# Optimization experiments

Hardware: AMD Instinct MI355X
Metric: run time of the kernel (lower is better)

Reference implementation:

```python
import jax, jax.numpy as jnp
import numpy as np

DIM = 2048
N_HEADS = 32
N_KV_HEADS = 8
HEAD_DIM = 64
REPEATS = N_HEADS // N_KV_HEADS
SCALE = HEAD_DIM ** -0.5
L = 2048
B = 1


def rotary_matrix(context_len, d):
    # Dense (L, d, d) RoPE rotation matrix, exactly as get_rotary_matrix1.
    pos = jnp.arange(1, context_len + 1, dtype=jnp.float32)[:, None]
    i = jnp.arange(d // 2)
    theta = 10000.0 ** (-2.0 * i.astype(jnp.float32) / d)
    m_theta = pos * theta  # (L, d/2)
    cos_v, sin_v = jnp.cos(m_theta), jnp.sin(m_theta)
    R = jnp.zeros((context_len, d, d), dtype=jnp.float32)
    R = R.at[:, 2 * i, 2 * i].set(cos_v)
    R = R.at[:, 2 * i, 2 * i + 1].set(-sin_v)
    R = R.at[:, 2 * i + 1, 2 * i].set(sin_v)
    R = R.at[:, 2 * i + 1, 2 * i + 1].set(cos_v)
    return R


def causal_mask(context_len):
    idx = jnp.arange(context_len)
    return (idx[:, None] < idx[None, :]).astype(jnp.float32) * -1e9


def setup_inputs() -> dict:
    key = jax.random.key(0)
    ks = jax.random.split(key, 5)
    x = jax.random.normal(ks[0], (B, L, DIM), dtype=jnp.float32)
    mask = causal_mask(L)
    wq_w = jax.random.normal(ks[1], (N_HEADS * HEAD_DIM, DIM), dtype=jnp.float32) * 0.02
    wk_w = jax.random.normal(ks[2], (N_KV_HEADS * HEAD_DIM, DIM), dtype=jnp.float32) * 0.02
    wv_w = jax.random.normal(ks[3], (N_KV_HEADS * HEAD_DIM, DIM), dtype=jnp.float32) * 0.02
    wo_w = jax.random.normal(ks[4], (DIM, N_HEADS * HEAD_DIM), dtype=jnp.float32) * 0.02
    return {"x": x, "mask": mask, "wq_w": wq_w, "wk_w": wk_w, "wv_w": wv_w, "wo_w": wo_w}


def reference(x, mask, wq_w, wk_w, wv_w, wo_w):
    Bx, Lx, D = x.shape
    # projections (torch Linear: y = x @ W.T)
    q = jnp.einsum('bld,od->blo', x, wq_w).reshape(Bx, Lx, N_HEADS, HEAD_DIM).transpose(0, 2, 1, 3)
    k = jnp.einsum('bld,od->blo', x, wk_w).reshape(Bx, Lx, N_KV_HEADS, HEAD_DIM).transpose(0, 2, 1, 3)
    v = jnp.einsum('bld,od->blo', x, wv_w).reshape(Bx, Lx, N_KV_HEADS, HEAD_DIM).transpose(0, 2, 1, 3)
    # GQA repeat of kv heads (interleaved, matching concat-unsqueeze-reshape)
    k = jnp.repeat(k, REPEATS, axis=1)
    v = jnp.repeat(v, REPEATS, axis=1)
    # dense-matrix RoPE on q and (repeated) k
    R = rotary_matrix(Lx, HEAD_DIM)
    q = jnp.einsum('bhlj,lij->bhli', q, R)
    k = jnp.einsum('bhlj,lij->bhli', k, R)
    scores = jnp.einsum('bhld,bhmd->bhlm', q, k) * SCALE + mask
    attn = jax.nn.softmax(scores.astype(jnp.float32), axis=-1)
    out = jnp.einsum('bhlm,bhmd->bhld', attn, v)
    out = out.transpose(0, 2, 1, 3).reshape(Bx, Lx, N_HEADS * HEAD_DIM)
    out = jnp.einsum('blo,do->bld', out, wo_w)
    return out, k, v
```

## Files before the change

### kernel.cpp

```cpp
#include <hip/hip_runtime.h>

typedef __bf16 bf16;
typedef __bf16 bf16x8 __attribute__((ext_vector_type(8)));
typedef float floatx4 __attribute__((ext_vector_type(4)));
typedef float floatx16 __attribute__((ext_vector_type(16)));
typedef unsigned int uint;

#define MFMA16(a, b, c) __builtin_amdgcn_mfma_f32_16x16x32_bf16((a), (b), (c), 0, 0, 0)
#define MFMA32(a, b, c) __builtin_amdgcn_mfma_f32_32x32x16_bf16((a), (b), (c), 0, 0, 0)

__device__ __forceinline__ void gl2lds16(const bf16* g, bf16* l) {
  __builtin_amdgcn_global_load_lds(
      (const __attribute__((address_space(1))) void*)g,
      (__attribute__((address_space(3))) void*)l, 16, 0, 0);
}
__device__ __forceinline__ void wait_vm0() { __builtin_amdgcn_s_waitcnt(0x0f70); }

__device__ __forceinline__ float* slot_ptr(int s, float* o0, float* o1) {
  return s < 512 ? o0 + (size_t)s * 8192 : o1 + (size_t)(s - 512) * 8192;
}
__device__ __forceinline__ const float* slot_ptr_c(int s, const float* o0,
                                                   const float* o1) {
  return s < 512 ? o0 + (size_t)s * 8192 : o1 + (size_t)(s - 512) * 8192;
}

__device__ __forceinline__ void cvt8(const float* __restrict__ s,
                                     bf16* __restrict__ d, int i8) {
  const float4 a = ((const float4*)s)[i8 * 2];
  const float4 b = ((const float4*)s)[i8 * 2 + 1];
  bf16x8 o;
  o[0] = (bf16)a.x; o[1] = (bf16)a.y; o[2] = (bf16)a.z; o[3] = (bf16)a.w;
  o[4] = (bf16)b.x; o[5] = (bf16)b.y; o[6] = (bf16)b.z; o[7] = (bf16)b.w;
  *(bf16x8*)(d + i8 * 8) = o;
}

__global__ __launch_bounds__(256) void convert_kernel(
    const float* __restrict__ x, const float* __restrict__ wq,
    const float* __restrict__ wk, const float* __restrict__ wv,
    bf16* __restrict__ xb, bf16* __restrict__ wqb, bf16* __restrict__ wkb,
    bf16* __restrict__ wvb) {
  const int g = blockIdx.x * 256 + threadIdx.x;
  if (g < 524288) cvt8(x, xb, g);
  else if (g < 1048576) cvt8(wq, wqb, g - 524288);
  else if (g < 1179648) cvt8(wk, wkb, g - 1048576);
  else cvt8(wv, wvb, g - 1179648);
}

template <typename OutT>
__device__ __forceinline__ void gemm_tile_body64(
    const bf16* __restrict__ A, int lda,
    const bf16* __restrict__ B, int ldb,
    OutT* __restrict__ C, int ldc, int K,
    bf16* S) {
  const int t = threadIdx.x;
  const int w = t >> 6, lane = t & 63;
  const int l15 = lane & 15, qd = lane >> 4;
  const int wr = w >> 1, wc = w & 1;

  floatx4 acc[2][4];
#pragma unroll
  for (int i = 0; i < 2; ++i)
#pragma unroll
    for (int j = 0; j < 4; ++j) acc[i][j] = (floatx4){0.f, 0.f, 0.f, 0.f};

  const bf16* gb[6];
  int lo[6];
#pragma unroll
  for (int i = 0; i < 6; ++i) {
    const int u = w + 4 * i;
    lo[i] = u * 512 + lane * 8;
    if (u < 8) {
      gb[i] = A + ((u >> 1) * 16 + l15) * lda + (u & 1) * 32 + qd * 8;
    } else {
      const int v = u - 8;
      gb[i] = B + ((v >> 1) * 16 + l15) * ldb + (v & 1) * 32 + qd * 8;
    }
  }

#define STG64(kt_, buf_)                                            \
  {                                                                 \
    bf16* d_ = S + (buf_) * 12288;                                  \
    _Pragma("unroll")                                               \
    for (int i_ = 0; i_ < 6; ++i_)                                  \
      gl2lds16(gb[i_] + (kt_) * 64, d_ + lo[i_]);                   \
  }

  const int NT = K >> 6;
  STG64(0, 0);
  wait_vm0();
  __syncthreads();
  int cur = 0;
  for (int kt = 0; kt < NT; ++kt) {
    if (kt + 1 < NT) STG64(kt + 1, cur ^ 1);
    const bf16* Ab = S + cur * 12288;
    const bf16* Bb = Ab + 4096;
    bf16x8 a[2][2], b[4][2];
#pragma unroll
    for (int i = 0; i < 2; ++i)
#pragma unroll
      for (int kk = 0; kk < 2; ++kk)
        a[i][kk] =
            *(const bf16x8*)(Ab + ((wr * 2 + i) * 2 + kk) * 512 + lane * 8);
#pragma unroll
    for (int j = 0; j < 4; ++j)
#pragma unroll
      for (int kk = 0; kk < 2; ++kk)
        b[j][kk] =
            *(const bf16x8*)(Bb + ((wc * 4 + j) * 2 + kk) * 512 + lane * 8);
#pragma unroll
    for (int kk = 0; kk < 2; ++kk)
#pragma unroll
      for (int i = 0; i < 2; ++i)
#pragma unroll
        for (int j = 0; j < 4; ++j)
          acc[i][j] = MFMA16(a[i][kk], b[j][kk], acc[i][j]);
    wait_vm0();
    __builtin_amdgcn_sched_barrier(0);
    __builtin_amdgcn_s_barrier();
    __builtin_amdgcn_sched_barrier(0);
    cur ^= 1;
  }
#undef STG64

#pragma unroll
  for (int i = 0; i < 2; ++i)
#pragma unroll
    for (int j = 0; j < 4; ++j) {
      const int row = wr * 32 + i * 16 + qd * 4;
      const int col = wc * 64 + j * 16 + l15;
#pragma unroll
      for (int r = 0; r < 4; ++r)
        C[(row + r) * ldc + col] = (OutT)acc[i][j][r];
    }
}

__global__ __launch_bounds__(256) void gemm_qkv(
    const bf16* __restrict__ x, const bf16* __restrict__ wq,
    const bf16* __restrict__ wk, const bf16* __restrict__ wv,
    bf16* __restrict__ Qws, bf16* __restrict__ Kh, bf16* __restrict__ Vh,
    bf16* __restrict__ Vt) {
  __shared__ bf16 SM[17152];
  bf16* As = SM;
  bf16* Bs = SM + 8192;
  const int bid = blockIdx.y * 24 + blockIdx.x;
  const int swz = (bid & 7) * 48 + (bid >> 3);
  const int nb = swz % 24;
  const int m0 = (swz / 24) * 128;
  const bf16* B;
  if (nb < 16) B = wq + nb * 128 * 2048;
  else if (nb < 20) B = wk + (nb - 16) * 128 * 2048;
  else B = wv + (nb - 20) * 128 * 2048;

  const int t = threadIdx.x;
  const int w = t >> 6, lane = t & 63;
  const int l15 = lane & 15, qd = lane >> 4;
  const int wr = w >> 1, wc = w & 1;

  floatx4 acc[4][4];
#pragma unroll
  for (int i = 0; i < 4; ++i)
#pragma unroll
    for (int j = 0; j < 4; ++j) acc[i][j] = (floatx4){0.f, 0.f, 0.f, 0.f};

  const bf16* A = x + m0 * 2048;
  const int mt0 = w, mt1 = w + 4;
  const int kseg = qd * 8;
  const bf16* ga0 = A + (mt0 * 16 + l15) * 2048 + kseg;
  const bf16* ga1 = A + (mt1 * 16 + l15) * 2048 + kseg;
  const bf16* gb0 = B + (mt0 * 16 + l15) * 2048 + kseg;
  const bf16* gb1 = B + (mt1 * 16 + l15) * 2048 + kseg;
  bf16* lA00 = As + (mt0 * 2 + 0) * 512 + lane * 8;
  bf16* lA01 = As + (mt0 * 2 + 1) * 512 + lane * 8;
  bf16* lA10 = As + (mt1 * 2 + 0) * 512 + lane * 8;
  bf16* lA11 = As + (mt1 * 2 + 1) * 512 + lane * 8;
  bf16* lB00 = Bs + (mt0 * 2 + 0) * 512 + lane * 8;
  bf16* lB01 = Bs + (mt0 * 2 + 1) * 512 + lane * 8;
  bf16* lB10 = Bs + (mt1 * 2 + 0) * 512 + lane * 8;
  bf16* lB11 = Bs + (mt1 * 2 + 1) * 512 + lane * 8;

  for (int k0 = 0; k0 < 2048; k0 += 64) {
    gl2lds16(ga0 + k0, lA00);
    gl2lds16(ga0 + k0 + 32, lA01);
    gl2lds16(ga1 + k0, lA10);
    gl2lds16(ga1 + k0 + 32, lA11);
    gl2lds16(gb0 + k0, lB00);
    gl2lds16(gb0 + k0 + 32, lB01);
    gl2lds16(gb1 + k0, lB10);
    gl2lds16(gb1 + k0 + 32, lB11);
    wait_vm0();
    __syncthreads();

    bf16x8 a[4][2], b[4][2];
#pragma unroll
    for (int i = 0; i < 4; ++i)
#pragma unroll
      for (int kk = 0; kk < 2; ++kk)
        a[i][kk] =
            *(const bf16x8*)(As + ((wr * 4 + i) * 2 + kk) * 512 + lane * 8);
#pragma unroll
    for (int j = 0; j < 4; ++j)
#pragma unroll
      for (int kk = 0; kk < 2; ++kk)
        b[j][kk] =
            *(const bf16x8*)(Bs + ((wc * 4 + j) * 2 + kk) * 512 + lane * 8);
#pragma unroll
    for (int kk = 0; kk < 2; ++kk)
#pragma unroll
      for (int i = 0; i < 4; ++i)
#pragma unroll
        for (int j = 0; j < 4; ++j)
          acc[i][j] = MFMA16(a[i][kk], b[j][kk], acc[i][j]);
    __syncthreads();
  }

#pragma unroll
  for (int i = 0; i < 4; ++i)
#pragma unroll
    for (int j = 0; j < 4; ++j) {
      const int row = wr * 64 + i * 16 + qd * 4;
      const int col = wc * 64 + j * 16 + l15;
#pragma unroll
      for (int r = 0; r < 4; ++r)
        SM[(row + r) * 134 + col] = (bf16)acc[i][j][r];
    }
  __syncthreads();

  const float NEG_LOG2_10000_D32 = -0.4152410118609203f;
  if (nb < 16) {
#pragma unroll
    for (int k = 0; k < 8; ++k) {
      const int u = t + (k << 8);
      const int row = u >> 4, c8 = (u & 15) << 3;
      const bf16x8 v = *(const bf16x8*)&SM[row * 134 + c8];
      const float base = (float)(m0 + row + 1);
      bf16x8 ov;
#pragma unroll
      for (int p = 0; p < 4; ++p) {
        const int a = ((c8 & 63) >> 1) + p;
        float s, c;
        __sincosf(base * exp2f(NEG_LOG2_10000_D32 * (float)a), &s, &c);
        const float x0 = (float)v[2 * p], x1 = (float)v[2 * p + 1];
        ov[2 * p] = (bf16)(c * x0 - s * x1);
        ov[2 * p + 1] = (bf16)(s * x0 + c * x1);
      }
      *(bf16x8*)&Qws[(m0 + row) * 2048 + nb * 128 + c8] = ov;
    }
  } else if (nb < 20) {
#pragma unroll
    for (int k = 0; k < 8; ++k) {
      const int u = t + (k << 8);
      const int row = u >> 4, c8 = (u & 15) << 3;
      const bf16x8 v = *(const bf16x8*)&SM[row * 134 + c8];
      const float base = (float)(m0 + row + 1);
      bf16x8 ov;
#pragma unroll
      for (int p = 0; p < 4; ++p) {
        const int a = ((c8 & 63) >> 1) + p;
        float s, c;
        __sincosf(base * exp2f(NEG_LOG2_10000_D32 * (float)a), &s, &c);
        const float x0 = (float)v[2 * p], x1 = (float)v[2 * p + 1];
        ov[2 * p] = (bf16)(c * x0 - s * x1);
        ov[2 * p + 1] = (bf16)(s * x0 + c * x1);
      }
      const int g512 = (nb - 16) * 128 + c8;
      const int kvh = g512 >> 6, d8 = g512 & 63;
      *(bf16x8*)&Kh[(kvh * 2048 + m0 + row) * 64 + d8] = ov;
    }
  } else {
#pragma unroll
    for (int k = 0; k < 8; ++k) {
      const int u = t + (k << 8);
      const int row = u >> 4, c8 = (u & 15) << 3;
      const bf16x8 v = *(const bf16x8*)&SM[row * 134 + c8];
      const int g512 = (nb - 20) * 128 + c8;
      const int kvh = g512 >> 6, d8 = g512 & 63;
      *(bf16x8*)&Vh[(kvh * 2048 + m0 + row) * 64 + d8] = v;
    }
#pragma unroll
    for (int k = 0; k < 8; ++k) {
      const int u = t + (k << 8);
      const int col = u >> 4, r8 = (u & 15) << 3;
      bf16x8 v;
#pragma unroll
      for (int jj = 0; jj < 8; ++jj) v[jj] = SM[(r8 + jj) * 134 + col];
      const int g512 = (nb - 20) * 128 + col;
      const int kvh = g512 >> 6, d = g512 & 63;
      *(bf16x8*)&Vt[kvh * 131072 + d * 2048 + m0 + r8] = v;
    }
  }
}

__global__ __launch_bounds__(256) void gemm_o(
    const bf16* __restrict__ Ows, const bf16* __restrict__ wo,
    float* __restrict__ out, const bf16* __restrict__ Kh,
    const bf16* __restrict__ Vh, float* __restrict__ kout,
    float* __restrict__ vout) {
  __shared__ bf16 S[24576];
  const int bid = blockIdx.y * 16 + blockIdx.x;
  const int swz = (bid & 7) * 64 + (bid >> 3);
  const int n0 = (swz & 15) * 128;
  const int m0 = (swz >> 4) * 64;
  gemm_tile_body64<float>(Ows + m0 * 2048, 2048, wo + n0 * 2048, 2048,
                          out + m0 * 2048 + n0, 2048, 2048, S);

  const int g = bid * 256 + (int)threadIdx.x;
  for (uint u = (uint)g; u < 262144u; u += 131072u) {
    const uint u2 = u & 131071u;
    const bf16* src = (u < 131072u) ? Kh : Vh;
    float* dst = (u < 131072u) ? kout : vout;
    const int kvh2 = u2 >> 14;
    const int rr = u2 & 16383;
    const int l = rr >> 3, d8 = (rr & 7) * 8;
    const bf16x8 v = *(const bf16x8*)(src + (kvh2 * 2048 + l) * 64 + d8);
    float4 f0, f1;
    f0.x = (float)v[0]; f0.y = (float)v[1]; f0.z = (float)v[2]; f0.w = (float)v[3];
    f1.x = (float)v[4]; f1.y = (float)v[5]; f1.z = (float)v[6]; f1.w = (float)v[7];
#pragma unroll
    for (int rep = 0; rep < 4; ++rep) {
      float* o2 = dst + (((kvh2 * 4 + rep) * 2048 + l) * 64 + d8);
      *(float4*)o2 = f0;
      *(float4*)(o2 + 4) = f1;
    }
  }
}

__global__ __launch_bounds__(256) void flash_kernel(
    const bf16* __restrict__ Qws, const bf16* __restrict__ Kh,
    const bf16* __restrict__ Vt, bf16* __restrict__ Ows,
    float* __restrict__ Op0, float* __restrict__ Op1, float* __restrict__ ML,
    const float* __restrict__ wo, bf16* __restrict__ wob) {
  __shared__ bf16 SMEM[16384];

  const int h = blockIdx.y;
  const int bx = 35 - (int)blockIdx.x;
  int qt, seg, kts, kte, slot;
  if (bx < 4) {
    qt = bx; seg = -1; kts = 0; kte = 2 * qt + 2; slot = -1;
  } else if (bx < 12) {
    const int j = bx - 4;
    qt = 4 + (j >> 1); seg = j & 1;
    const int nkt = 2 * qt + 2;
    kts = seg * nkt / 2; kte = (seg + 1) * nkt / 2;
    slot = h * 32 + (bx - 4);
  } else {
    const int j = bx - 12;
    qt = 8 + j / 3; seg = j % 3;
    const int nkt = 2 * qt + 2;
    kts = seg * nkt / 3; kte = (seg + 1) * nkt / 3;
    slot = h * 32 + (bx - 4);
  }
  const int kh = h >> 2;
  const int q0 = qt * 128;
  const int t = threadIdx.x, w = t >> 6, lane = t & 63;
  const int l31 = lane & 31, hf = lane >> 5;
  const int qw = q0 + w * 32;

  const int s0 = w, s1 = w + 4;
  const bf16* gK0 = Kh + kh * 131072 + ((s0 >> 2) * 32 + l31) * 64 + (s0 & 3) * 16 + hf * 8;
  const bf16* gK1 = Kh + kh * 131072 + ((s1 >> 2) * 32 + l31) * 64 + (s1 & 3) * 16 + hf * 8;
  const bf16* gV0 = Vt + kh * 131072 + ((s0 >> 2) * 32 + l31) * 2048 + (s0 & 3) * 16 + hf * 8;
  const bf16* gV1 = Vt + kh * 131072 + ((s1 >> 2) * 32 + l31) * 2048 + (s1 & 3) * 16 + hf * 8;

  {
    const int nb = kts & 1;
    gl2lds16(gK0 + kts * 4096, &SMEM[nb * 8192 + s0 * 512 + lane * 8]);
    gl2lds16(gK1 + kts * 4096, &SMEM[nb * 8192 + s1 * 512 + lane * 8]);
    gl2lds16(gV0 + kts * 64, &SMEM[nb * 8192 + 4096 + s0 * 512 + lane * 8]);
    gl2lds16(gV1 + kts * 64, &SMEM[nb * 8192 + 4096 + s1 * 512 + lane * 8]);
  }

  bf16x8 qf[4];
  {
    const bf16* qrow = Qws + (qw + l31) * 2048 + h * 64 + hf * 8;
#pragma unroll
    for (int c = 0; c < 4; ++c) qf[c] = *(const bf16x8*)(qrow + c * 16);
  }

  floatx16 o[2] = {};
  float mrun = -3e38f, lrun = 0.f;

  const float C = 0.1803368801f;
  for (int kt = kts; kt < kte; ++kt) {
    wait_vm0();
    __syncthreads();
    if (kt + 1 < kte) {
      const int nb = (kt + 1) & 1;
      const int koff = (kt + 1) * 4096, voff = (kt + 1) * 64;
      gl2lds16(gK0 + koff, &SMEM[nb * 8192 + s0 * 512 + lane * 8]);
      gl2lds16(gK1 + koff, &SMEM[nb * 8192 + s1 * 512 + lane * 8]);
      gl2lds16(gV0 + voff, &SMEM[nb * 8192 + 4096 + s0 * 512 + lane * 8]);
      gl2lds16(gV1 + voff, &SMEM[nb * 8192 + 4096 + s1 * 512 + lane * 8]);
    }
    const int kt64 = kt * 64;
    if (kt64 > qw + 31) continue;
    const bf16* Kb = &SMEM[(kt & 1) * 8192];
    const bf16* Vb = Kb + 4096;

    floatx16 st[2];
    __builtin_amdgcn_s_setprio(1);
#pragma unroll
    for (int tt = 0; tt < 2; ++tt) {
      floatx16 z = {};
#pragma unroll
      for (int c = 0; c < 4; ++c) {
        const bf16x8 kf = *(const bf16x8*)(Kb + (tt * 4 + c) * 512 + lane * 8);
        z = MFMA32(kf, qf[c], z);
      }
      st[tt] = z;
    }
    __builtin_amdgcn_s_setprio(0);
    if (kt64 + 64 > qw) {
      const int myq = qw + l31;
#pragma unroll
      for (int tt = 0; tt < 2; ++tt)
#pragma unroll
        for (int r = 0; r < 16; ++r) {
          const int key = kt64 + tt * 32 + (r & 3) + 8 * (r >> 2) + 4 * hf;
          if (key > myq) st[tt][r] = -1e30f;
        }
    }
    float ma = -3e38f, mb = -3e38f, mc = -3e38f, md = -3e38f;
#pragma unroll
    for (int tt = 0; tt < 2; ++tt)
#pragma unroll
      for (int r = 0; r < 16; r += 4) {
        ma = fmaxf(ma, st[tt][r + 0]);
        mb = fmaxf(mb, st[tt][r + 1]);
        mc = fmaxf(mc, st[tt][r + 2]);
        md = fmaxf(md, st[tt][r + 3]);
      }
    float mx = fmaxf(fmaxf(ma, mb), fmaxf(mc, md));
    mx = fmaxf(mx, __shfl_xor(mx, 32));
    const bool defer = __all((mx - mrun) * C <= 8.f);
    if (!defer) {
      const float mn = fmaxf(mrun, mx);
      const float al = __builtin_amdgcn_exp2f((mrun - mn) * C);
      lrun *= al;
#pragma unroll
      for (int n = 0; n < 2; ++n)
#pragma unroll
        for (int r = 0; r < 16; ++r) o[n][r] *= al;
      mrun = mn;
    }
    float ra = 0.f, rb = 0.f, rc = 0.f, rd = 0.f;
#pragma unroll
    for (int tt = 0; tt < 2; ++tt)
#pragma unroll
      for (int r = 0; r < 16; r += 4) {
        const float p0 = __builtin_amdgcn_exp2f((st[tt][r + 0] - mrun) * C);
        const float p1 = __builtin_amdgcn_exp2f((st[tt][r + 1] - mrun) * C);
        const float p2 = __builtin_amdgcn_exp2f((st[tt][r + 2] - mrun) * C);
        const float p3 = __builtin_amdgcn_exp2f((st[tt][r + 3] - mrun) * C);
        st[tt][r + 0] = p0; ra += p0;
        st[tt][r + 1] = p1; rb += p1;
        st[tt][r + 2] = p2; rc += p2;
        st[tt][r + 3] = p3; rd += p3;
      }
    float rs = (ra + rb) + (rc + rd);
    rs += __shfl_xor(rs, 32);
    lrun += rs;

    uint pk[2][4][2];
#pragma unroll
    for (int tt = 0; tt < 2; ++tt)
#pragma unroll
      for (int g = 0; g < 4; ++g)
#pragma unroll
        for (int p = 0; p < 2; ++p) {
          union { bf16 h2[2]; uint u; } cv;
          cv.h2[0] = (bf16)st[tt][4 * g + 2 * p];
          cv.h2[1] = (bf16)st[tt][4 * g + 2 * p + 1];
          pk[tt][g][p] = cv.u;
        }
    uint own_[2][2][2], rv[2][2][2];
#pragma unroll
    for (int tt = 0; tt < 2; ++tt)
#pragma unroll
      for (int gam = 0; gam < 2; ++gam)
#pragma unroll
        for (int p = 0; p < 2; ++p) {
          own_[tt][gam][p] = hf ? pk[tt][2 * gam + 1][p] : pk[tt][2 * gam][p];
          const uint snd = hf ? pk[tt][2 * gam][p] : pk[tt][2 * gam + 1][p];
          rv[tt][gam][p] = (uint)__shfl_xor((int)snd, 32);
        }
    __builtin_amdgcn_s_setprio(1);
#pragma unroll
    for (int c = 0; c < 4; ++c) {
      const int tt = c >> 1, gam = c & 1;
      union { uint u[4]; bf16x8 v; } pf;
      pf.u[0] = hf ? rv[tt][gam][0] : own_[tt][gam][0];
      pf.u[1] = hf ? rv[tt][gam][1] : own_[tt][gam][1];
      pf.u[2] = hf ? own_[tt][gam][0] : rv[tt][gam][0];
      pf.u[3] = hf ? own_[tt][gam][1] : rv[tt][gam][1];
#pragma unroll
      for (int n = 0; n < 2; ++n)
        o[n] = MFMA32(*(const bf16x8*)(Vb + (n * 4 + c) * 512 + lane * 8),
                      pf.v, o[n]);
    }
    __builtin_amdgcn_s_setprio(0);
  }

  if (seg < 0) {
    __syncthreads();
    bf16* Osh = SMEM;
    const float inv = 1.f / lrun;
#pragma unroll
    for (int n = 0; n < 2; ++n)
#pragma unroll
      for (int r = 0; r < 16; ++r) {
        const int dl = n * 32 + (r & 3) + 8 * (r >> 2) + 4 * hf;
        Osh[(w * 32 + l31) * 66 + dl] = (bf16)(o[n][r] * inv);
      }
    __syncthreads();
#pragma unroll
    for (int i = 0; i < 4; ++i) {
      const int row = (t >> 3) + i * 32;
      const int col = (t & 7) * 8;
      const bf16x8 vv = *(const bf16x8*)&Osh[row * 66 + col];
      *(bf16x8*)&Ows[(q0 + row) * 2048 + h * 64 + col] = vv;
    }
  } else {
    float* Op = slot_ptr(slot, Op0, Op1);
#pragma unroll
    for (int n = 0; n < 2; ++n)
#pragma unroll
      for (int r = 0; r < 16; ++r) {
        const int dl = n * 32 + (r & 3) + 8 * (r >> 2) + 4 * hf;
        Op[dl * 128 + w * 32 + l31] = o[n][r];
      }
    if (hf == 0) {
      ML[slot * 256 + w * 32 + l31] = mrun;
      ML[slot * 256 + 128 + w * 32 + l31] = lrun;
    }
  }

  {
    const int bidf = (int)blockIdx.y * 36 + (int)blockIdx.x;
    for (uint u = (uint)(bidf * 256 + t); u < 524288u; u += 294912u)
      cvt8(wo, wob, (int)u);
  }
}

__global__ __launch_bounds__(256) void combine_kernel(
    const float* __restrict__ Op0, const float* __restrict__ Op1,
    const float* __restrict__ ML, bf16* __restrict__ Ows) {
  __shared__ bf16 Osh[128 * 66];
  const int b = blockIdx.x;
  const int h = b / 12, qi = b % 12;
  const int qt = 4 + qi;
  const int q0 = qt * 128;
  const bool three = (qi >= 4);
  const int slot0 = h * 32 + (three ? 8 + (qi - 4) * 3 : qi * 2);
  const int t = threadIdx.x;
  const int row = t & 127, dh = t >> 7;
  const float C = 0.1803368801f;
  const float m0 = ML[(slot0 + 0) * 256 + row], l0 = ML[(slot0 + 0) * 256 + 128 + row];
  const float m1 = ML[(slot0 + 1) * 256 + row], l1 = ML[(slot0 + 1) * 256 + 128 + row];
  const float m2 = three ? ML[(slot0 + 2) * 256 + row] : -3e38f;
  const float l2 = three ? ML[(slot0 + 2) * 256 + 128 + row] : 0.f;
  const float m = fmaxf(fmaxf(m0, m1), m2);
  const float w0 = __builtin_amdgcn_exp2f((m0 - m) * C);
  const float w1 = __builtin_amdgcn_exp2f((m1 - m) * C);
  const float w2 = three ? __builtin_amdgcn_exp2f((m2 - m) * C) : 0.f;
  const float inv = 1.f / (l0 * w0 + l1 * w1 + l2 * w2);
  const float* P0 = slot_ptr_c(slot0 + 0, Op0, Op1);
  const float* P1 = slot_ptr_c(slot0 + 1, Op0, Op1);
  const float* P2 = three ? slot_ptr_c(slot0 + 2, Op0, Op1) : P0;
#pragma unroll
  for (int j = 0; j < 32; ++j) {
    const int d = dh * 32 + j;
    const float v = (P0[d * 128 + row] * w0 + P1[d * 128 + row] * w1 +
                     P2[d * 128 + row] * w2) *
                    inv;
    Osh[row * 66 + d] = (bf16)v;
  }
  __syncthreads();
#pragma unroll
  for (int i = 0; i < 4; ++i) {
    const int r2 = (t >> 3) + i * 32;
    const int col = (t & 7) * 8;
    const bf16x8 vv = *(const bf16x8*)&Osh[r2 * 66 + col];
    *(bf16x8*)&Ows[(q0 + r2) * 2048 + h * 64 + col] = vv;
  }
}

extern "C" void kernel_launch(void* const* d_in, const int* in_sizes, int n_in,
                              void* d_out, int out_size, void* d_ws,
                              size_t ws_size, hipStream_t stream) {
  const float* x = (const float*)d_in[0];
  const float* wq = (const float*)d_in[2];
  const float* wk = (const float*)d_in[3];
  const float* wv = (const float*)d_in[4];
  const float* wo = (const float*)d_in[5];

  float* out = (float*)d_out;
  float* kout = out + 4194304;
  float* vout = out + 8388608;

  bf16* ws = (bf16*)d_ws;
  bf16* xb = ws;
  bf16* wqb = xb + 4194304;
  bf16* wkb = wqb + 4194304;
  bf16* wvb = wkb + 1048576;
  bf16* wob = wvb + 1048576;
  bf16* Qws = wob + 4194304;
  bf16* Kws = Qws + 4194304;
  bf16* Vh = Kws + 1048576;
  bf16* Vt = Vh + 1048576;
  bf16* Ows = Vt + 1048576;
  bf16* Kh = Ows + 4194304;
  float* Op0 = out;
  float* Op1 = (float*)ws;
  float* MLf = (float*)Kws;

  convert_kernel<<<dim3(5120), dim3(256), 0, stream>>>(x, wq, wk, wv, xb, wqb,
                                                       wkb, wvb);
  gemm_qkv<<<dim3(24, 16), dim3(256), 0, stream>>>(xb, wqb, wkb, wvb, Qws, Kh,
                                                   Vh, Vt);
  flash_kernel<<<dim3(36, 32), dim3(256), 0, stream>>>(Qws, Kh, Vt, Ows, Op0,
                                                       Op1, MLf, wo, wob);
  combine_kernel<<<dim3(384), dim3(256), 0, stream>>>(Op0, Op1, MLf, Ows);
  gemm_o<<<dim3(16, 32), dim3(256), 0, stream>>>(Ows, wob, out, Kh, Vh, kout,
                                                 vout);
}
```

Before: 277.9 us.

## Fuse split-K combine into flash kernel via last-block atomic counter

Removes the separate combine kernel: each split segment block increments a per-(head, query tile) atomic counter after writing its partial output and max/sum stats. The last block to arrive reads all partials and writes the normalized bf16 output. Counters are reset in the convert kernel. This saves a kernel launch and the gap between kernels, at the cost of threadfences, an atomic, and serial combine work in the tail blocks.

```diff
diff --git a/kernel.cpp b/kernel.cpp
--- a/kernel.cpp
+++ b/kernel.cpp
@@ -38,12 +38,15 @@
     const float* __restrict__ x, const float* __restrict__ wq,
     const float* __restrict__ wk, const float* __restrict__ wv,
     bf16* __restrict__ xb, bf16* __restrict__ wqb, bf16* __restrict__ wkb,
-    bf16* __restrict__ wvb) {
+    bf16* __restrict__ wvb, uint* __restrict__ cnt) {
   const int g = blockIdx.x * 256 + threadIdx.x;
   if (g < 524288) cvt8(x, xb, g);
   else if (g < 1048576) cvt8(wq, wqb, g - 524288);
   else if (g < 1179648) cvt8(wk, wkb, g - 1048576);
   else cvt8(wv, wvb, g - 1179648);
+  if (blockIdx.x == 0) {
+    for (int i = threadIdx.x; i < 384; i += 256) cnt[i] = 0u;
+  }
 }
 
 template <typename OutT>
@@ -328,23 +331,25 @@
     const bf16* __restrict__ Qws, const bf16* __restrict__ Kh,
     const bf16* __restrict__ Vt, bf16* __restrict__ Ows,
     float* __restrict__ Op0, float* __restrict__ Op1, float* __restrict__ ML,
-    const float* __restrict__ wo, bf16* __restrict__ wob) {
+    uint* __restrict__ cnt, const float* __restrict__ wo,
+    bf16* __restrict__ wob) {
   __shared__ bf16 SMEM[16384];
+  __shared__ int s_last;
 
   const int h = blockIdx.y;
   const int bx = 35 - (int)blockIdx.x;
-  int qt, seg, kts, kte, slot;
+  int qt, seg, kts, kte, slot, nseg;
   if (bx < 4) {
-    qt = bx; seg = -1; kts = 0; kte = 2 * qt + 2; slot = -1;
+    qt = bx; seg = -1; kts = 0; kte = 2 * qt + 2; slot = -1; nseg = 1;
   } else if (bx < 12) {
     const int j = bx - 4;
-    qt = 4 + (j >> 1); seg = j & 1;
+    qt = 4 + (j >> 1); seg = j & 1; nseg = 2;
     const int nkt = 2 * qt + 2;
     kts = seg * nkt / 2; kte = (seg + 1) * nkt / 2;
     slot = h * 32 + (bx - 4);
   } else {
     const int j = bx - 12;
-    qt = 8 + j / 3; seg = j % 3;
+    qt = 8 + j / 3; seg = j % 3; nseg = 3;
     const int nkt = 2 * qt + 2;
     kts = seg * nkt / 3; kte = (seg + 1) * nkt / 3;
     slot = h * 32 + (bx - 4);
@@ -532,55 +537,59 @@
       ML[slot * 256 + w * 32 + l31] = mrun;
       ML[slot * 256 + 128 + w * 32 + l31] = lrun;
     }
+
+    const int qi = qt - 4;
+    const int cidx = h * 12 + qi;
+    __threadfence();
+    __syncthreads();
+    if (t == 0) {
+      const uint old = atomicAdd(&cnt[cidx], 1u);
+      s_last = (old == (uint)(nseg - 1)) ? 1 : 0;
+    }
+    __syncthreads();
+    if (s_last) {
+      __threadfence();
+      const bool three = (nseg == 3);
+      const int slot0 = h * 32 + (three ? 8 + qi * 3 - 12 : qi * 2);
+      const int row = t & 127, dh = t >> 7;
+      const float m0_ = ML[(slot0 + 0) * 256 + row];
+      const float l0_ = ML[(slot0 + 0) * 256 + 128 + row];
+      const float m1_ = ML[(slot0 + 1) * 256 + row];
+      const float l1_ = ML[(slot0 + 1) * 256 + 128 + row];
+      const float m2_ = three ? ML[(slot0 + 2) * 256 + row] : -3e38f;
+      const float l2_ = three ? ML[(slot0 + 2) * 256 + 128 + row] : 0.f;
+      const float m = fmaxf(fmaxf(m0_, m1_), m2_);
+      const float w0_ = __builtin_amdgcn_exp2f((m0_ - m) * C);
+      const float w1_ = __builtin_amdgcn_exp2f((m1_ - m) * C);
+      const float w2_ = three ? __builtin_amdgcn_exp2f((m2_ - m) * C) : 0.f;
+      const float inv = 1.f / (l0_ * w0_ + l1_ * w1_ + l2_ * w2_);
+      const float* P0 = slot_ptr_c(slot0 + 0, Op0, Op1);
+      const float* P1 = slot_ptr_c(slot0 + 1, Op0, Op1);
+      const float* P2 = three ? slot_ptr_c(slot0 + 2, Op0, Op1) : P0;
+      bf16* Osh = SMEM;
+#pragma unroll
+      for (int j = 0; j < 32; ++j) {
+        const int d = dh * 32 + j;
+        const float v = (P0[d * 128 + row] * w0_ + P1[d * 128 + row] * w1_ +
+                         P2[d * 128 + row] * w2_) *
+                        inv;
+        Osh[row * 66 + d] = (bf16)v;
+      }
+      __syncthreads();
+#pragma unroll
+      for (int i = 0; i < 4; ++i) {
+        const int r2 = (t >> 3) + i * 32;
+        const int col = (t & 7) * 8;
+        const bf16x8 vv = *(const bf16x8*)&Osh[r2 * 66 + col];
+        *(bf16x8*)&Ows[(q0 + r2) * 2048 + h * 64 + col] = vv;
+      }
+    }
   }
 
   {
     const int bidf = (int)blockIdx.y * 36 + (int)blockIdx.x;
     for (uint u = (uint)(bidf * 256 + t); u < 524288u; u += 294912u)
       cvt8(wo, wob, (int)u);
-  }
-}
-
-__global__ __launch_bounds__(256) void combine_kernel(
-    const float* __restrict__ Op0, const float* __restrict__ Op1,
-    const float* __restrict__ ML, bf16* __restrict__ Ows) {
-  __shared__ bf16 Osh[128 * 66];
-  const int b = blockIdx.x;
-  const int h = b / 12, qi = b % 12;
-  const int qt = 4 + qi;
-  const int q0 = qt * 128;
-  const bool three = (qi >= 4);
-  const int slot0 = h * 32 + (three ? 8 + (qi - 4) * 3 : qi * 2);
-  const int t = threadIdx.x;
-  const int row = t & 127, dh = t >> 7;
-  const float C = 0.1803368801f;
-  const float m0 = ML[(slot0 + 0) * 256 + row], l0 = ML[(slot0 + 0) * 256 + 128 + row];
-  const float m1 = ML[(slot0 + 1) * 256 + row], l1 = ML[(slot0 + 1) * 256 + 128 + row];
-  const float m2 = three ? ML[(slot0 + 2) * 256 + row] : -3e38f;
-  const float l2 = three ? ML[(slot0 + 2) * 256 + 128 + row] : 0.f;
-  const float m = fmaxf(fmaxf(m0, m1), m2);
-  const float w0 = __builtin_amdgcn_exp2f((m0 - m) * C);
-  const float w1 = __builtin_amdgcn_exp2f((m1 - m) * C);
-  const float w2 = three ? __builtin_amdgcn_exp2f((m2 - m) * C) : 0.f;
-  const float inv = 1.f / (l0 * w0 + l1 * w1 + l2 * w2);
-  const float* P0 = slot_ptr_c(slot0 + 0, Op0, Op1);
-  const float* P1 = slot_ptr_c(slot0 + 1, Op0, Op1);
-  const float* P2 = three ? slot_ptr_c(slot0 + 2, Op0, Op1) : P0;
-#pragma unroll
-  for (int j = 0; j < 32; ++j) {
-    const int d = dh * 32 + j;
-    const float v = (P0[d * 128 + row] * w0 + P1[d * 128 + row] * w1 +
-                     P2[d * 128 + row] * w2) *
-                    inv;
-    Osh[row * 66 + d] = (bf16)v;
-  }
-  __syncthreads();
-#pragma unroll
-  for (int i = 0; i < 4; ++i) {
-    const int r2 = (t >> 3) + i * 32;
-    const int col = (t & 7) * 8;
-    const bf16x8 vv = *(const bf16x8*)&Osh[r2 * 66 + col];
-    *(bf16x8*)&Ows[(q0 + r2) * 2048 + h * 64 + col] = vv;
   }
 }
 
@@ -612,14 +621,14 @@
   float* Op0 = out;
   float* Op1 = (float*)ws;
   float* MLf = (float*)Kws;
+  uint* cnt = (uint*)(MLf + 262144);
 
   convert_kernel<<<dim3(5120), dim3(256), 0, stream>>>(x, wq, wk, wv, xb, wqb,
-                                                       wkb, wvb);
+                                                       wkb, wvb, cnt);
   gemm_qkv<<<dim3(24, 16), dim3(256), 0, stream>>>(xb, wqb, wkb, wvb, Qws, Kh,
                                                    Vh, Vt);
   flash_kernel<<<dim3(36, 32), dim3(256), 0, stream>>>(Qws, Kh, Vt, Ows, Op0,
-                                                       Op1, MLf, wo, wob);
-  combine_kernel<<<dim3(384), dim3(256), 0, stream>>>(Op0, Op1, MLf, Ows);
+                                                       Op1, MLf, cnt, wo, wob);
   gemm_o<<<dim3(16, 32), dim3(256), 0, stream>>>(Ows, wob, out, Kh, Vh, kout,
                                                  vout);
 }
```

After: 521.4 us. +87.6%, slower.
